# Kernel tuning notes

Hardware: AMD Instinct MI355X
Metric: run time of the kernel (lower is better)

Reference implementation:

```python
import jax, jax.numpy as jnp
import numpy as np

N = 100000          # number of nodes (queries == sources here)
DEG = 32            # uniform neighbor count
E = N * DEG         # total edges
C_IN = 8
HID = 32
C_OUT = 32


def setup_inputs() -> dict:
    key = jax.random.key(0)
    k1, k2, k3, k4, k5 = jax.random.split(key, 5)
    in_features = jax.random.normal(k1, (N, C_IN), dtype=jnp.float32)
    in_weights = jax.random.uniform(k2, (N,), dtype=jnp.float32)
    # MLP: Linear(2*C_IN -> HID), GELU, Linear(HID -> C_OUT)
    W1 = jax.random.normal(k3, (2 * C_IN, HID), dtype=jnp.float32) / np.sqrt(2 * C_IN)
    b1 = jnp.zeros((HID,), dtype=jnp.float32)
    W2 = jax.random.normal(k4, (HID, C_OUT), dtype=jnp.float32) / np.sqrt(HID)
    b2 = jnp.zeros((C_OUT,), dtype=jnp.float32)
    neighbor_index = jax.random.randint(k5, (E,), 0, N, dtype=jnp.int64)
    row_splits = (jnp.arange(N + 1, dtype=jnp.int64) * DEG)  # uniform CSR splits
    return {"in_features": in_features, "in_weights": in_weights,
            "W1": W1, "b1": b1, "W2": W2, "b2": b2,
            "neighbor_index": neighbor_index, "row_splits": row_splits}


def reference(in_features, in_weights, W1, b1, W2, b2, neighbor_index, row_splits):
    num_edges = neighbor_index.shape[0]
    num_out = row_splits.shape[0] - 1  # M output nodes
    # segment id of each edge (== repeat_interleave of node ids by row counts)
    seg = jnp.searchsorted(row_splits, jnp.arange(num_edges), side="right") - 1
    gathered = in_features[neighbor_index]          # [E, C_in] neighbor gather
    self_feats = in_features[seg]                   # [E, C_in] repeated self features
    agg = jnp.concatenate([gathered, self_feats], axis=1)  # [E, 2*C_in]
    h = jax.nn.gelu(agg @ W1 + b1)                  # [E, HID]
    h = h @ W2 + b2                                 # [E, C_out]
    h = in_weights[neighbor_index][:, None] * h     # quadrature weighting
    sums = jax.ops.segment_sum(h, seg, num_segments=num_out)  # segment_csr sum
    counts = (row_splits[1:] - row_splits[:-1]).astype(h.dtype)
    out = sums / jnp.maximum(counts, 1)[:, None]    # reduce='mean'
    return out
```

## Files before the change

kernel.cpp:

```cpp
#include <hip/hip_runtime.h>

#define DEG 32
#define HID 32
#define CIN 8

typedef float v2f __attribute__((ext_vector_type(2)));
typedef short bf16x8 __attribute__((ext_vector_type(8)));
typedef float f32x16 __attribute__((ext_vector_type(16)));

#define GELU_A ((float)(2.0 * 1.4426950408889634 * 0.7978845608028654))
#define GELU_B ((float)(2.0 * 1.4426950408889634 * 0.7978845608028654 * 0.044715))

__device__ __forceinline__ unsigned f2bf(float f) {
    unsigned b = __float_as_uint(f);
    return (b + 0x7fffu + ((b >> 16) & 1u)) >> 16;
}
__device__ __forceinline__ unsigned pack2(float lo, float hi) {
    return f2bf(lo) | (f2bf(hi) << 16);
}

__global__ __launch_bounds__(256) void precompute_xw(
    const float* __restrict__ x, const float* __restrict__ W1,
    const float* __restrict__ W2, unsigned* __restrict__ x16,
    unsigned* __restrict__ w1f, unsigned* __restrict__ w2f, int N) {
    int tid = blockIdx.x * 256 + threadIdx.x;
    if (blockIdx.x == 0) {
        int t = threadIdx.x;
        if (t < 64) {
            int kb = (t >> 5) * 8, col = t & 31;
            uint4 o;
            o.x = pack2(W1[(kb + 0) * HID + col], W1[(kb + 1) * HID + col]);
            o.y = pack2(W1[(kb + 2) * HID + col], W1[(kb + 3) * HID + col]);
            o.z = pack2(W1[(kb + 4) * HID + col], W1[(kb + 5) * HID + col]);
            o.w = pack2(W1[(kb + 6) * HID + col], W1[(kb + 7) * HID + col]);
            *(uint4*)(w1f + t * 4) = o;
        } else if (t < 192) {
            int u = t - 64;
            int f = u >> 6, l = u & 63;
            int kb = f * 16 + ((l >> 5) * 8), col = l & 31;
            uint4 o;
            o.x = pack2(W2[(kb + 0) * HID + col], W2[(kb + 1) * HID + col]);
            o.y = pack2(W2[(kb + 2) * HID + col], W2[(kb + 3) * HID + col]);
            o.z = pack2(W2[(kb + 4) * HID + col], W2[(kb + 5) * HID + col]);
            o.w = pack2(W2[(kb + 6) * HID + col], W2[(kb + 7) * HID + col]);
            *(uint4*)(w2f + (f * 64 + l) * 4) = o;
        }
    }
    if (tid < N) {
        const float4* xp = (const float4*)(x + (size_t)tid * CIN);
        float4 a = xp[0], b = xp[1];
        uint4 o;
        o.x = pack2(a.x, a.y);  o.y = pack2(a.z, a.w);
        o.z = pack2(b.x, b.y);  o.w = pack2(b.z, b.w);
        *(uint4*)(x16 + (size_t)tid * 4) = o;
    }
}

__device__ __forceinline__ float gelu_reduce(const f32x16& acc, const float* swp,
                                             float b1v) {
    v2f gacc = {0.f, 0.f};
#pragma unroll
    for (int q = 0; q < 4; ++q) {
        float4 wq = *(const float4*)(swp + 8 * q);
#pragma unroll
        for (int h = 0; h < 2; ++h) {
            int i = q * 4 + h * 2;
            v2f tt = {acc[i] + b1v, acc[i + 1] + b1v};
            v2f x2 = tt * tt;
            v2f zz = tt * (x2 * (-GELU_B) + (-GELU_A));
            v2f ee;
            ee.x = __builtin_amdgcn_exp2f(zz.x);  ee.y = __builtin_amdgcn_exp2f(zz.y);
            v2f dd = ee + 1.0f;
            v2f rr;
            rr.x = __builtin_amdgcn_rcpf(dd.x);   rr.y = __builtin_amdgcn_rcpf(dd.y);
            v2f wp = h ? (v2f){wq.z, wq.w} : (v2f){wq.x, wq.y};
            gacc += wp * (tt * rr);
        }
    }
    float g = gacc.x + gacc.y;
    g += __shfl_xor(g, 32);
    return g;
}

__global__ __launch_bounds__(256) void git_fused_g(
    const unsigned* __restrict__ x16, const unsigned* __restrict__ w1f,
    const float* __restrict__ wgt, const float* __restrict__ b1,
    const int* __restrict__ nbr, unsigned short* __restrict__ gws,
    float* __restrict__ wsum, int N) {
    __shared__ float sw[4 * 64];

    int t = threadIdx.x;
    int wv = t >> 6;
    int l  = t & 63;
    int l5 = l & 31;
    int hi = l >> 5;
    int nb = blockIdx.x * 8 + wv * 2;

    int n0 = min(nb + 0, N - 1), n1 = min(nb + 1, N - 1);

    int   J = nbr[(hi ? n1 : n0) * DEG + l5];
    float W = wgt[J];
    int jsw = __shfl_xor(J, 32);

    const bf16x8* x16v = (const bf16x8*)x16;
    bf16x8 A0 = x16v[hi ? n0 : J];
    bf16x8 A1 = x16v[hi ? n1 : jsw];
    bf16x8 bfrag = *((const bf16x8*)w1f + l);
    float myb1 = b1[l5];

    float* swv = &sw[wv * 64];
    swv[hi * 32 + l5] = W;

    float ws = W;
    ws += __shfl_xor(ws, 1);  ws += __shfl_xor(ws, 2);
    ws += __shfl_xor(ws, 4);  ws += __shfl_xor(ws, 8);
    ws += __shfl_xor(ws, 16);

    f32x16 z0 = {}, z1 = {};
    f32x16 a0 = __builtin_amdgcn_mfma_f32_32x32x16_bf16(A0, bfrag, z0, 0, 0, 0);
    f32x16 a1 = __builtin_amdgcn_mfma_f32_32x32x16_bf16(A1, bfrag, z1, 0, 0, 0);

    float g0 = gelu_reduce(a0, swv + hi * 4,      myb1);
    float g1 = gelu_reduce(a1, swv + 32 + hi * 4, myb1);

    float ga   = hi ? g1 : g0;
    int   node = hi ? n1 : n0;
    gws[(size_t)node * HID + l5] = (unsigned short)f2bf(ga);
    if (l5 == 0) wsum[node] = ws;
}

__global__ __launch_bounds__(256) void git_w2(
    const unsigned short* __restrict__ gws, const unsigned* __restrict__ w2f,
    const float* __restrict__ wsum, const float* __restrict__ b2,
    float* __restrict__ out, int N) {
    __shared__ float sws[4 * 32];

    int t = threadIdx.x;
    int wv = t >> 6, l = t & 63, l5 = l & 31, hi = l >> 5;
    int nb = blockIdx.x * 128 + wv * 32;
    int nl = min(nb + l5, N - 1);

    const char* gb = (const char*)gws;
    bf16x8 ea1 = *(const bf16x8*)(gb + (size_t)nl * 64 + hi * 16);
    bf16x8 ea2 = *(const bf16x8*)(gb + (size_t)nl * 64 + 32 + hi * 16);
    bf16x8 eb1 = *((const bf16x8*)w2f + l);
    bf16x8 eb2 = *((const bf16x8*)w2f + 64 + l);
    sws[wv * 32 + l5] = wsum[nl];
    float myb2 = b2[l5];

    f32x16 zz = {};
    f32x16 acc = __builtin_amdgcn_mfma_f32_32x32x16_bf16(ea1, eb1, zz, 0, 0, 0);
    acc = __builtin_amdgcn_mfma_f32_32x32x16_bf16(ea2, eb2, acc, 0, 0, 0);

    const float* swsv = &sws[wv * 32];
#pragma unroll
    for (int i = 0; i < 16; ++i) {
        int r = (i & 3) + 8 * (i >> 2) + 4 * hi;
        int node = nb + r;
        if (node < N)
            out[(size_t)node * HID + l5] = fmaf(swsv[r], myb2, acc[i]) * (1.0f / DEG);
    }
}

__global__ __launch_bounds__(256) void fused_fallback(
    const float* __restrict__ x, const float* __restrict__ wgt,
    const float* __restrict__ W1, const float* __restrict__ b1,
    const float* __restrict__ W2, const float* __restrict__ b2,
    const int* __restrict__ nbr, float* __restrict__ out, int N) {
    __shared__ float sW2[HID * HID];
    __shared__ float sb2[HID];
    __shared__ int2  sp[8 * DEG];
    int t = threadIdx.x;
#pragma unroll
    for (int i = 0; i < 4; ++i) sW2[t + i * 256] = W2[t + i * 256];
    if (t < HID) sb2[t] = b2[t];
    int slot = t >> 5, hid = t & 31;
    int node = blockIdx.x * 8 + slot;
    bool valid = node < N;
    int nc = valid ? node : (N - 1);
    int   j_own = nbr[nc * DEG + hid];
    float w_own = wgt[j_own];
    sp[slot * DEG + hid] = make_int2(j_own * (CIN * 4), __float_as_int(w_own));
    const float4* xip = (const float4*)(x + (size_t)nc * CIN);
    float4 xa = xip[0], xb = xip[1];
    float w1t[8];
#pragma unroll
    for (int k = 0; k < 8; ++k) w1t[k] = W1[k * HID + hid];
    float vb = b1[hid];
    vb = fmaf(xa.x, W1[ 8 * HID + hid], vb);
    vb = fmaf(xa.y, W1[ 9 * HID + hid], vb);
    vb = fmaf(xa.z, W1[10 * HID + hid], vb);
    vb = fmaf(xa.w, W1[11 * HID + hid], vb);
    vb = fmaf(xb.x, W1[12 * HID + hid], vb);
    vb = fmaf(xb.y, W1[13 * HID + hid], vb);
    vb = fmaf(xb.z, W1[14 * HID + hid], vb);
    vb = fmaf(xb.w, W1[15 * HID + hid], vb);
    float ws = w_own;
    ws += __shfl_xor(ws, 1);  ws += __shfl_xor(ws, 2);
    ws += __shfl_xor(ws, 4);  ws += __shfl_xor(ws, 8);
    ws += __shfl_xor(ws, 16);
    __syncthreads();
    const char* xbytes = (const char*)x;
    const int2* myp = &sp[slot * DEG];
    float g = 0.f;
#pragma unroll 8
    for (int e = 0; e < DEG; ++e) {
        int2  p  = myp[e];
        float wjv = __int_as_float(p.y);
        const float4* xjp = (const float4*)(xbytes + (unsigned)p.x);
        float4 a = xjp[0], b = xjp[1];
        float tin = vb;
        tin = fmaf(a.x, w1t[0], tin); tin = fmaf(a.y, w1t[1], tin);
        tin = fmaf(a.z, w1t[2], tin); tin = fmaf(a.w, w1t[3], tin);
        tin = fmaf(b.x, w1t[4], tin); tin = fmaf(b.y, w1t[5], tin);
        tin = fmaf(b.z, w1t[6], tin); tin = fmaf(b.w, w1t[7], tin);
        float x2 = tin * tin;
        float z  = tin * fmaf(GELU_B, x2, GELU_A);
        float e2 = __builtin_amdgcn_exp2f(z);
        float r  = __builtin_amdgcn_rcpf(1.0f + e2);
        g = fmaf(wjv, fmaf(-tin, r, tin), g);
    }
    float acc = 0.f;
#pragma unroll
    for (int h = 0; h < HID; ++h) {
        float gh = __shfl(g, h, 32);
        acc = fmaf(gh, sW2[h * HID + hid], acc);
    }
    if (valid) out[(size_t)node * HID + hid] = fmaf(ws, sb2[hid], acc) * (1.0f / DEG);
}

extern "C" void kernel_launch(void* const* d_in, const int* in_sizes, int n_in,
                              void* d_out, int out_size, void* d_ws, size_t ws_size,
                              hipStream_t stream) {
    const float* x   = (const float*)d_in[0];
    const float* wq  = (const float*)d_in[1];
    const float* W1  = (const float*)d_in[2];
    const float* b1  = (const float*)d_in[3];
    const float* W2  = (const float*)d_in[4];
    const float* b2  = (const float*)d_in[5];
    const int*   nbr = (const int*)d_in[6];
    float* out = (float*)d_out;

    int N = in_sizes[1];

    size_t off_x16  = 0;
    size_t off_w1   = (off_x16 + (size_t)N * 16 + 255) & ~(size_t)255;
    size_t off_w2   = off_w1 + 1024;
    size_t off_g    = (off_w2 + 2048 + 255) & ~(size_t)255;
    size_t off_wsum = (off_g + (size_t)N * HID * 2 + 255) & ~(size_t)255;
    size_t need     = off_wsum + (size_t)N * 4;

    if (ws_size >= need) {
        unsigned* x16 = (unsigned*)((char*)d_ws + off_x16);
        unsigned* w1f = (unsigned*)((char*)d_ws + off_w1);
        unsigned* w2f = (unsigned*)((char*)d_ws + off_w2);
        unsigned short* gws = (unsigned short*)((char*)d_ws + off_g);
        float* wsum = (float*)((char*)d_ws + off_wsum);

        int blocks_pre = (N + 255) / 256;
        precompute_xw<<<blocks_pre, 256, 0, stream>>>(x, W1, W2, x16, w1f, w2f, N);

        int blocks_main = (N + 7) / 8;
        git_fused_g<<<blocks_main, 256, 0, stream>>>(x16, w1f, wq, b1, nbr,
                                                     gws, wsum, N);

        int blocks_ep = (N + 127) / 128;
        git_w2<<<blocks_ep, 256, 0, stream>>>(gws, w2f, wsum, b2, out, N);
    } else {
        int blocks = (N + 7) / 8;
        fused_fallback<<<blocks, 256, 0, stream>>>(x, wq, W1, b1, W2, b2, nbr, out, N);
    }
}
```

Measured before the change: 120.6 us.

## Fuse W2 epilogue into main gather kernel through per-wave LDS staging

Removes the separate git_w2 kernel and the global gws/wsum intermediates. Each wave now stages its two nodes' GELU-reduced hidden vectors in LDS and runs the W2 MFMA right there, writing final outputs directly. This saves a kernel launch and a global write/read round trip, at the cost of a mostly wasted 32x32 MFMA per wave, since only two rows are real. Block size also doubles to 512 threads with launch bounds adjusted.

```diff
diff --git a/kernel.cpp b/kernel.cpp
--- a/kernel.cpp
+++ b/kernel.cpp
@@ -82,19 +82,20 @@
     return g;
 }
 
-__global__ __launch_bounds__(256) void git_fused_g(
+__global__ __launch_bounds__(512, 4) void git_fused(
     const unsigned* __restrict__ x16, const unsigned* __restrict__ w1f,
-    const float* __restrict__ wgt, const float* __restrict__ b1,
-    const int* __restrict__ nbr, unsigned short* __restrict__ gws,
-    float* __restrict__ wsum, int N) {
-    __shared__ float sw[4 * 64];
+    const unsigned* __restrict__ w2f, const float* __restrict__ wgt,
+    const float* __restrict__ b1, const float* __restrict__ b2,
+    const int* __restrict__ nbr, float* __restrict__ out, int N) {
+    __shared__ float sw[8 * 64];
+    __shared__ __align__(16) unsigned short sg[2432];
 
     int t = threadIdx.x;
     int wv = t >> 6;
     int l  = t & 63;
     int l5 = l & 31;
     int hi = l >> 5;
-    int nb = blockIdx.x * 8 + wv * 2;
+    int nb = blockIdx.x * 16 + wv * 2;
 
     int n0 = min(nb + 0, N - 1), n1 = min(nb + 1, N - 1);
 
@@ -123,42 +124,26 @@
     float g0 = gelu_reduce(a0, swv + hi * 4,      myb1);
     float g1 = gelu_reduce(a1, swv + 32 + hi * 4, myb1);
 
-    float ga   = hi ? g1 : g0;
-    int   node = hi ? n1 : n0;
-    gws[(size_t)node * HID + l5] = (unsigned short)f2bf(ga);
-    if (l5 == 0) wsum[node] = ws;
-}
-
-__global__ __launch_bounds__(256) void git_w2(
-    const unsigned short* __restrict__ gws, const unsigned* __restrict__ w2f,
-    const float* __restrict__ wsum, const float* __restrict__ b2,
-    float* __restrict__ out, int N) {
-    __shared__ float sws[4 * 32];
-
-    int t = threadIdx.x;
-    int wv = t >> 6, l = t & 63, l5 = l & 31, hi = l >> 5;
-    int nb = blockIdx.x * 128 + wv * 32;
-    int nl = min(nb + l5, N - 1);
-
-    const char* gb = (const char*)gws;
-    bf16x8 ea1 = *(const bf16x8*)(gb + (size_t)nl * 64 + hi * 16);
-    bf16x8 ea2 = *(const bf16x8*)(gb + (size_t)nl * 64 + 32 + hi * 16);
+    unsigned short* sgw = &sg[wv * 160];
+    float ga = hi ? g1 : g0;
+    sgw[hi * 40 + l5] = (unsigned short)f2bf(ga);
+
     bf16x8 eb1 = *((const bf16x8*)w2f + l);
     bf16x8 eb2 = *((const bf16x8*)w2f + 64 + l);
-    sws[wv * 32 + l5] = wsum[nl];
     float myb2 = b2[l5];
-
+    const char* sgb = (const char*)sgw;
+    bf16x8 ea1 = *(const bf16x8*)(sgb + l5 * 80 + hi * 16);
+    bf16x8 ea2 = *(const bf16x8*)(sgb + l5 * 80 + 32 + hi * 16);
     f32x16 zz = {};
     f32x16 acc = __builtin_amdgcn_mfma_f32_32x32x16_bf16(ea1, eb1, zz, 0, 0, 0);
     acc = __builtin_amdgcn_mfma_f32_32x32x16_bf16(ea2, eb2, acc, 0, 0, 0);
 
-    const float* swsv = &sws[wv * 32];
-#pragma unroll
-    for (int i = 0; i < 16; ++i) {
-        int r = (i & 3) + 8 * (i >> 2) + 4 * hi;
-        int node = nb + r;
-        if (node < N)
-            out[(size_t)node * HID + l5] = fmaf(swsv[r], myb2, acc[i]) * (1.0f / DEG);
+    float wsx = __shfl_xor(ws, 32);
+    if (hi == 0) {
+        if (nb < N)
+            out[(size_t)n0 * HID + l5] = fmaf(ws,  myb2, acc[0]) * (1.0f / DEG);
+        if (nb + 1 < N)
+            out[(size_t)n1 * HID + l5] = fmaf(wsx, myb2, acc[1]) * (1.0f / DEG);
     }
 }
 
@@ -243,29 +228,22 @@
 
     int N = in_sizes[1];
 
-    size_t off_x16  = 0;
-    size_t off_w1   = (off_x16 + (size_t)N * 16 + 255) & ~(size_t)255;
-    size_t off_w2   = off_w1 + 1024;
-    size_t off_g    = (off_w2 + 2048 + 255) & ~(size_t)255;
-    size_t off_wsum = (off_g + (size_t)N * HID * 2 + 255) & ~(size_t)255;
-    size_t need     = off_wsum + (size_t)N * 4;
+    size_t off_x16 = 0;
+    size_t off_w1  = (off_x16 + (size_t)N * 16 + 255) & ~(size_t)255;
+    size_t off_w2  = off_w1 + 1024;
+    size_t need    = off_w2 + 2048;
 
     if (ws_size >= need) {
         unsigned* x16 = (unsigned*)((char*)d_ws + off_x16);
         unsigned* w1f = (unsigned*)((char*)d_ws + off_w1);
         unsigned* w2f = (unsigned*)((char*)d_ws + off_w2);
-        unsigned short* gws = (unsigned short*)((char*)d_ws + off_g);
-        float* wsum = (float*)((char*)d_ws + off_wsum);
 
         int blocks_pre = (N + 255) / 256;
         precompute_xw<<<blocks_pre, 256, 0, stream>>>(x, W1, W2, x16, w1f, w2f, N);
 
-        int blocks_main = (N + 7) / 8;
-        git_fused_g<<<blocks_main, 256, 0, stream>>>(x16, w1f, wq, b1, nbr,
-                                                     gws, wsum, N);
-
-        int blocks_ep = (N + 127) / 128;
-        git_w2<<<blocks_ep, 256, 0, stream>>>(gws, w2f, wsum, b2, out, N);
+        int blocks_main = (N + 15) / 16;
+        git_fused<<<blocks_main, 512, 0, stream>>>(x16, w1f, w2f, wq, b1, b2,
+                                                   nbr, out, N);
     } else {
         int blocks = (N + 7) / 8;
         fused_fallback<<<blocks, 256, 0, stream>>>(x, wq, W1, b1, W2, b2, nbr, out, N);
```

Measured after the change: 114.9 us. -4.7%, faster.
